# Kernel tuning notes

Hardware: AMD Instinct MI355X
Metric: run time of the kernel (lower is better)

Reference implementation:

```python
import jax, jax.numpy as jnp
import numpy as np

N_NODES = 10000
N_EDGES = 160000
MUL = 64            # multiplicity of 0e and 1o in node features
AVG_NEIGH = 16.0    # avg_num_neighbors
N_BESSEL = 8
NUM_IRREPS = 4 * MUL  # 2*MUL scalars (0e) + 2*MUL vectors (1o) after concat+regroup

# e3nn normalize2mom constant for swish: 1/sqrt(E_{z~N(0,1)}[swish(z)^2])
_z, _w = np.polynomial.hermite_e.hermegauss(128)
_silu = _z / (1.0 + np.exp(-_z))
ACT_C = float(1.0 / np.sqrt(np.sum(_w * _silu ** 2) / np.sqrt(2.0 * np.pi)))


def bessel(x, n=N_BESSEL):
    # e3nn.bessel with x_max=1: sqrt(2) * sin(k*pi*x)/x, k=1..n
    k = jnp.arange(1, n + 1, dtype=x.dtype)
    xs = jnp.where(x == 0.0, 1.0, x)[:, None]
    return jnp.sqrt(2.0) * jnp.where(x[:, None] == 0.0, k * jnp.pi, jnp.sin(jnp.pi * k * xs) / xs)


def envelope(x):
    return jnp.where(x < 1.0, 1.0 - 28.0 * x ** 6 + 48.0 * x ** 7 - 21.0 * x ** 8, 0.0)


def mlp(x, Ws):
    # e3nn MultiLayerPerceptron: y = x @ W / sqrt(fan_in), normalized swish on hidden layers
    n = len(Ws)
    for i, W in enumerate(Ws):
        x = x @ W / jnp.sqrt(jnp.asarray(W.shape[0], x.dtype))
        if i < n - 1:
            x = ACT_C * jax.nn.swish(x)
    return x


def setup_inputs() -> dict:
    key = jax.random.key(0)
    ks = jax.random.split(key, 8)
    vectors = 0.35 * jax.random.normal(ks[0], (N_EDGES, 3), jnp.float32)
    node_scalars = jax.random.normal(ks[1], (N_NODES, MUL), jnp.float32)
    node_vectors = jax.random.normal(ks[2], (N_NODES, MUL, 3), jnp.float32)
    senders = jax.random.randint(ks[3], (N_EDGES,), 0, N_NODES)
    receivers = jax.random.randint(ks[4], (N_EDGES,), 0, N_NODES)
    W1 = jax.random.normal(ks[5], (N_BESSEL, 64), jnp.float32)
    W2 = jax.random.normal(ks[6], (64, 64), jnp.float32)
    W3 = jax.random.normal(ks[7], (64, NUM_IRREPS), jnp.float32)
    return dict(vectors=vectors, node_scalars=node_scalars, node_vectors=node_vectors,
                senders=senders, receivers=receivers, W1=W1, W2=W2, W3=W3)


def reference(vectors, node_scalars, node_vectors, senders, receivers, W1, W2, W3):
    lengths = jnp.linalg.norm(vectors, axis=-1, keepdims=True)        # [E,1]
    Y1 = jnp.sqrt(3.0) * vectors / lengths                            # component-normalized l=1 SH [E,3]

    # gather sender features
    m0 = node_scalars[senders]                                        # [E,MUL]   0e
    m1 = node_vectors[senders]                                        # [E,MUL,3] 1o

    # CG tensor product with Y1, filtered to target irreps (0e + 1o), component norm
    tp0 = jnp.einsum('eui,ei->eu', m1, Y1) / jnp.sqrt(3.0)            # 1o x 1o -> 0e
    tp1 = m0[:, :, None] * Y1[:, None, :]                             # 0e x 1o -> 1o

    s = jnp.concatenate([m0, tp0], axis=1)                            # [E,2*MUL]
    v = jnp.concatenate([m1, tp1], axis=1)                            # [E,2*MUL,3]

    # radial embedding -> per-irrep gates
    x = lengths[:, 0]
    radial = bessel(x) * envelope(x)[:, None]                         # [E,8]
    mix = mlp(radial, (W1, W2, W3))                                   # [E,4*MUL]

    s = s * mix[:, : 2 * MUL]
    v = v * mix[:, 2 * MUL :, None]

    # scatter-add to receivers
    out_s = jax.ops.segment_sum(s, receivers, num_segments=N_NODES)   # [N,2*MUL]
    out_v = jax.ops.segment_sum(v, receivers, num_segments=N_NODES)   # [N,2*MUL,3]
    inv = 1.0 / jnp.sqrt(AVG_NEIGH)
    return jnp.concatenate([out_s * inv, (out_v * inv).reshape(N_NODES, -1)], axis=1)
```

## Files before the change

### kernel.cpp

```cpp
#include <hip/hip_runtime.h>
#include <hip/hip_fp16.h>
#include <math.h>

#define N_NODES 10000
#define N_EDGES 160000
#define TBL_N 512
#define ACT_C 1.676518f
#define CAP 64
#define S3 1.7320508075688772f

#define SCAT_BLOCKS 625
#define CONV_BLOCKS 2500
#define TBL_BLOCKS  129

__device__ uint4  g_tblp[TBL_N * 64];
__device__ uint2  g_nd2[N_NODES * 64];
__device__ int    g_cnt[N_NODES];
__device__ float4 g_bkt[N_NODES * CAP];

__device__ __forceinline__ float2 h2f(unsigned int v) {
    __half2 h = *(__half2*)&v;
    return __half22float2(h);
}

__global__ __launch_bounds__(256) void prep_scatter(
    const float* __restrict__ W1, const float* __restrict__ W2, const float* __restrict__ W3,
    const float* __restrict__ node_scalars, const float* __restrict__ node_vectors,
    const float* __restrict__ vectors, const int* __restrict__ senders,
    const int* __restrict__ receivers)
{
    const int bx = (int)blockIdx.x;
    const int tid = threadIdx.x;
    const int lane = tid & 63;
    const int wl = tid >> 6;

    if (bx < SCAT_BLOCKS) {
        int e = bx * 256 + tid;
        if (e < N_EDGES) {
            float vx = vectors[3 * e], vy = vectors[3 * e + 1], vz = vectors[3 * e + 2];
            float x2 = vx * vx + vy * vy + vz * vz;
            if (x2 < 1.0f) {
                float invx = rsqrtf(x2);
                float x = x2 * invx;
                float t = x * (float)TBL_N;
                int idx = (int)t;            if (idx > TBL_N - 1) idx = TBL_N - 1;
                int fr  = (int)((t - (float)idx) * 512.0f);  if (fr > 511) fr = 511;
                unsigned int bits = ((unsigned int)senders[e] << 18) |
                                    ((unsigned int)idx << 9) | (unsigned int)fr;
                int r = receivers[e];
                int slot = atomicAdd(&g_cnt[r], 1);
                if (slot < CAP)
                    g_bkt[(r << 6) + slot] =
                        make_float4(vx * invx, vy * invx, vz * invx, __uint_as_float(bits));
            }
        }
        return;
    }
    if (bx < SCAT_BLOCKS + CONV_BLOCKS) {
        int n = (bx - SCAT_BLOCKS) * 4 + wl;
        float m0 = node_scalars[n * 64 + lane];
        const float* p = node_vectors + n * 192 + 3 * lane;
        __half2 h01 = __floats2half2_rn(m0, p[0]);
        __half2 h23 = __floats2half2_rn(p[1], p[2]);
        uint2 r;
        r.x = *(unsigned int*)&h01;
        r.y = *(unsigned int*)&h23;
        g_nd2[n * 64 + lane] = r;
        return;
    }

    __shared__ float h[4][64];
    int wid = (bx - SCAT_BLOCKS - CONV_BLOCKS) * 4 + wl;
    if (wid > TBL_N) wid = TBL_N;
    const float x = (float)wid * (1.0f / (float)TBL_N);
    float x2 = x * x, x3 = x2 * x, x6 = x3 * x3;
    float env = (x < 1.0f) ? (1.0f - 28.0f * x6 + 48.0f * x6 * x - 21.0f * x6 * x2) : 0.0f;
    const float pi = 3.14159265358979f;
    float radial[8];
    #pragma unroll
    for (int k = 1; k <= 8; ++k) {
        float b = (x == 0.0f) ? ((float)k * pi) : (sinf(pi * (float)k * x) / x);
        radial[k - 1] = 1.41421356237f * b * env;
    }
    float acc = 0.0f;
    #pragma unroll
    for (int k = 0; k < 8; ++k) acc += radial[k] * W1[k * 64 + lane];
    acc *= 0.35355339059f;
    float a = ACT_C * acc / (1.0f + expf(-acc));
    h[wl][lane] = a;
    __syncthreads();
    acc = 0.0f;
    #pragma unroll 8
    for (int k = 0; k < 64; ++k) acc += h[wl][k] * W2[k * 64 + lane];
    acc *= 0.125f;
    a = ACT_C * acc / (1.0f + expf(-acc));
    __syncthreads();
    h[wl][lane] = a;
    __syncthreads();
    float m0 = 0.f, m1 = 0.f, m2 = 0.f, m3 = 0.f;
    #pragma unroll 4
    for (int k = 0; k < 64; ++k) {
        float hk = h[wl][k];
        const float* w = W3 + k * 256 + lane;
        m0 += hk * w[0];
        m1 += hk * w[64];
        m2 += hk * w[128];
        m3 += hk * w[192];
    }
    __half2 h01 = __floats2half2_rn(m0 * 0.125f, m1 * 0.125f);
    __half2 h23 = __floats2half2_rn(m2 * 0.125f, m3 * 0.125f);
    uint2 r;
    r.x = *(unsigned int*)&h01;
    r.y = *(unsigned int*)&h23;
    if (wid < TBL_N) *(uint2*)&g_tblp[wid * 64 + lane] = r;
    if (wid >= 1)    *(uint2*)((char*)&g_tblp[(wid - 1) * 64 + lane] + 8) = r;
}

__device__ __forceinline__ void edge_body(int j, const float4& myrec,
                                          int u, float& accA, float& accB,
                                          float& aCx, float& aCy, float& aCz,
                                          float& aDx, float& aDy, float& aDz) {
    float yx = __shfl(myrec.x, j);
    float yy = __shfl(myrec.y, j);
    float yz = __shfl(myrec.z, j);
    unsigned int bits = __float_as_uint(__shfl(myrec.w, j));
    int sv = (int)(bits >> 18);
    int i  = (int)((bits >> 9) & 511u);
    float f = (float)(bits & 511u) * (1.0f / 512.0f);

    uint4 q  = g_tblp[i * 64 + u];
    uint2 nv = g_nd2[sv * 64 + u];

    float2 a0 = h2f(q.x);
    float2 b0 = h2f(q.y);
    float2 a1 = h2f(q.z);
    float2 b1 = h2f(q.w);
    float2 p01 = h2f(nv.x);
    float2 p23 = h2f(nv.y);

    float mA = fmaf(f, a1.x - a0.x, a0.x);
    float mB = fmaf(f, a1.y - a0.y, a0.y);
    float mC = fmaf(f, b1.x - b0.x, b0.x);
    float mD = fmaf(f, b1.y - b0.y, b0.y);

    float m0u = p01.x, vx = p01.y, vy = p23.x, vzv = p23.y;
    float tp0 = fmaf(vx, yx, fmaf(vy, yy, vzv * yz));
    accA = fmaf(m0u, mA, accA);
    accB = fmaf(tp0, mB, accB);
    aCx = fmaf(mC, vx,  aCx);
    aCy = fmaf(mC, vy,  aCy);
    aCz = fmaf(mC, vzv, aCz);
    float cD = m0u * mD * S3;
    aDx = fmaf(cD, yx, aDx);
    aDy = fmaf(cD, yy, aDy);
    aDz = fmaf(cD, yz, aDz);
}

__global__ __launch_bounds__(256) void gather_kernel(float* __restrict__ out) {
    __shared__ float smem[3][8][64];
    const int n = (int)blockIdx.x;
    const int u = threadIdx.x & 63;
    const int w = threadIdx.x >> 6;

    int cnt = g_cnt[n]; if (cnt > CAP) cnt = CAP;
    int ql = (cnt + 3) >> 2;
    int beg = w * ql;
    int len = cnt - beg; if (len > ql) len = ql; if (len < 0) len = 0;
    const int base = n << 6;
    const float4 myrec = g_bkt[base + beg + (u < len ? u : 0)];

    float accA = 0.f, accB = 0.f;
    float aCx = 0.f, aCy = 0.f, aCz = 0.f;
    float aDx = 0.f, aDy = 0.f, aDz = 0.f;
    int j = 0;
    for (; j + 2 <= len; j += 2) {
        edge_body(j,     myrec, u, accA, accB, aCx, aCy, aCz, aDx, aDy, aDz);
        edge_body(j + 1, myrec, u, accA, accB, aCx, aCy, aCz, aDx, aDy, aDz);
    }
    if (j < len)
        edge_body(j,     myrec, u, accA, accB, aCx, aCy, aCz, aDx, aDy, aDz);

    if (w > 0) {
        smem[w - 1][0][u] = accA;  smem[w - 1][1][u] = accB;
        smem[w - 1][2][u] = aCx;   smem[w - 1][3][u] = aCy;
        smem[w - 1][4][u] = aCz;   smem[w - 1][5][u] = aDx;
        smem[w - 1][6][u] = aDy;   smem[w - 1][7][u] = aDz;
    }
    __syncthreads();
    if (w == 0) {
        #pragma unroll
        for (int s = 0; s < 3; ++s) {
            accA += smem[s][0][u]; accB += smem[s][1][u];
            aCx  += smem[s][2][u]; aCy  += smem[s][3][u];
            aCz  += smem[s][4][u]; aDx  += smem[s][5][u];
            aDy  += smem[s][6][u]; aDz  += smem[s][7][u];
        }
        const float inv = 0.25f;
        float* o = out + (size_t)n * 512;
        o[u]       = inv * accA;
        o[64 + u]  = inv * accB;
        o[128 + 3 * u + 0] = inv * aCx;
        o[128 + 3 * u + 1] = inv * aCy;
        o[128 + 3 * u + 2] = inv * aCz;
        o[320 + 3 * u + 0] = inv * aDx;
        o[320 + 3 * u + 1] = inv * aDy;
        o[320 + 3 * u + 2] = inv * aDz;
    }
    if (threadIdx.x == 0) g_cnt[n] = 0;
}

extern "C" void kernel_launch(void* const* d_in, const int* in_sizes, int n_in,
                              void* d_out, int out_size, void* d_ws, size_t ws_size,
                              hipStream_t stream) {
    const float* vectors      = (const float*)d_in[0];
    const float* node_scalars = (const float*)d_in[1];
    const float* node_vectors = (const float*)d_in[2];
    const int*   senders      = (const int*)d_in[3];
    const int*   receivers    = (const int*)d_in[4];
    const float* W1           = (const float*)d_in[5];
    const float* W2           = (const float*)d_in[6];
    const float* W3           = (const float*)d_in[7];
    float* out = (float*)d_out;

    prep_scatter<<<SCAT_BLOCKS + CONV_BLOCKS + TBL_BLOCKS, 256, 0, stream>>>(
        W1, W2, W3, node_scalars, node_vectors, vectors, senders, receivers);
    gather_kernel<<<N_NODES, 256, 0, stream>>>(out);
}
```

Baseline: 43.60 us.

## Stage coarser radial table in LDS and gather nodes per wave persistently

Shrinks the radial-MLP interpolation table to 127 entries stored as plain uint2 and copies it into shared memory in each block of a persistent gather kernel. Each wave now handles one whole node, removing the cross-wave shared-memory reduction, and edge loads are batched four at a time to expose memory-level parallelism. Sender bits are repacked to fit the smaller index field. The trade-offs are coarser interpolation accuracy, a per-block table copy, and a large LDS footprint that limits occupancy.

After: 45.29 us. +3.9%, slower.

```diff
diff --git a/kernel.cpp b/kernel.cpp
--- a/kernel.cpp
+++ b/kernel.cpp
@@ -4,16 +4,18 @@
 
 #define N_NODES 10000
 #define N_EDGES 160000
-#define TBL_N 512
+#define TBL_N 126
 #define ACT_C 1.676518f
 #define CAP 64
 #define S3 1.7320508075688772f
 
 #define SCAT_BLOCKS 625
 #define CONV_BLOCKS 2500
-#define TBL_BLOCKS  129
-
-__device__ uint4  g_tblp[TBL_N * 64];
+#define TBL_BLOCKS  32
+#define GATHER_BLOCKS 512
+#define GATHER_THREADS 512
+
+__device__ uint2  g_tbl[(TBL_N + 1) * 64];
 __device__ uint2  g_nd2[N_NODES * 64];
 __device__ int    g_cnt[N_NODES];
 __device__ float4 g_bkt[N_NODES * CAP];
@@ -45,7 +47,7 @@
                 float t = x * (float)TBL_N;
                 int idx = (int)t;            if (idx > TBL_N - 1) idx = TBL_N - 1;
                 int fr  = (int)((t - (float)idx) * 512.0f);  if (fr > 511) fr = 511;
-                unsigned int bits = ((unsigned int)senders[e] << 18) |
+                unsigned int bits = ((unsigned int)senders[e] << 16) |
                                     ((unsigned int)idx << 9) | (unsigned int)fr;
                 int r = receivers[e];
                 int slot = atomicAdd(&g_cnt[r], 1);
@@ -112,29 +114,18 @@
     uint2 r;
     r.x = *(unsigned int*)&h01;
     r.y = *(unsigned int*)&h23;
-    if (wid < TBL_N) *(uint2*)&g_tblp[wid * 64 + lane] = r;
-    if (wid >= 1)    *(uint2*)((char*)&g_tblp[(wid - 1) * 64 + lane] + 8) = r;
-}
-
-__device__ __forceinline__ void edge_body(int j, const float4& myrec,
-                                          int u, float& accA, float& accB,
+    g_tbl[wid * 64 + lane] = r;
+}
+
+__device__ __forceinline__ void edge_math(uint2 q0, uint2 q1, uint2 nv, float f,
+                                          float yx, float yy, float yz,
+                                          float& accA, float& accB,
                                           float& aCx, float& aCy, float& aCz,
                                           float& aDx, float& aDy, float& aDz) {
-    float yx = __shfl(myrec.x, j);
-    float yy = __shfl(myrec.y, j);
-    float yz = __shfl(myrec.z, j);
-    unsigned int bits = __float_as_uint(__shfl(myrec.w, j));
-    int sv = (int)(bits >> 18);
-    int i  = (int)((bits >> 9) & 511u);
-    float f = (float)(bits & 511u) * (1.0f / 512.0f);
-
-    uint4 q  = g_tblp[i * 64 + u];
-    uint2 nv = g_nd2[sv * 64 + u];
-
-    float2 a0 = h2f(q.x);
-    float2 b0 = h2f(q.y);
-    float2 a1 = h2f(q.z);
-    float2 b1 = h2f(q.w);
+    float2 a0 = h2f(q0.x);
+    float2 b0 = h2f(q0.y);
+    float2 a1 = h2f(q1.x);
+    float2 b1 = h2f(q1.y);
     float2 p01 = h2f(nv.x);
     float2 p23 = h2f(nv.y);
 
@@ -156,45 +147,61 @@
     aDz = fmaf(cD, yz, aDz);
 }
 
-__global__ __launch_bounds__(256) void gather_kernel(float* __restrict__ out) {
-    __shared__ float smem[3][8][64];
-    const int n = (int)blockIdx.x;
-    const int u = threadIdx.x & 63;
-    const int w = threadIdx.x >> 6;
-
-    int cnt = g_cnt[n]; if (cnt > CAP) cnt = CAP;
-    int ql = (cnt + 3) >> 2;
-    int beg = w * ql;
-    int len = cnt - beg; if (len > ql) len = ql; if (len < 0) len = 0;
-    const int base = n << 6;
-    const float4 myrec = g_bkt[base + beg + (u < len ? u : 0)];
-
-    float accA = 0.f, accB = 0.f;
-    float aCx = 0.f, aCy = 0.f, aCz = 0.f;
-    float aDx = 0.f, aDy = 0.f, aDz = 0.f;
-    int j = 0;
-    for (; j + 2 <= len; j += 2) {
-        edge_body(j,     myrec, u, accA, accB, aCx, aCy, aCz, aDx, aDy, aDz);
-        edge_body(j + 1, myrec, u, accA, accB, aCx, aCy, aCz, aDx, aDy, aDz);
-    }
-    if (j < len)
-        edge_body(j,     myrec, u, accA, accB, aCx, aCy, aCz, aDx, aDy, aDz);
-
-    if (w > 0) {
-        smem[w - 1][0][u] = accA;  smem[w - 1][1][u] = accB;
-        smem[w - 1][2][u] = aCx;   smem[w - 1][3][u] = aCy;
-        smem[w - 1][4][u] = aCz;   smem[w - 1][5][u] = aDx;
-        smem[w - 1][6][u] = aDy;   smem[w - 1][7][u] = aDz;
-    }
-    __syncthreads();
-    if (w == 0) {
-        #pragma unroll
-        for (int s = 0; s < 3; ++s) {
-            accA += smem[s][0][u]; accB += smem[s][1][u];
-            aCx  += smem[s][2][u]; aCy  += smem[s][3][u];
-            aCz  += smem[s][4][u]; aDx  += smem[s][5][u];
-            aDy  += smem[s][6][u]; aDz  += smem[s][7][u];
+__global__ __launch_bounds__(GATHER_THREADS) void gather_kernel(float* __restrict__ out) {
+    __shared__ uint2 tbl[(TBL_N + 1) * 64];
+    const int tid = threadIdx.x;
+    for (int i = tid; i < (TBL_N + 1) * 64; i += GATHER_THREADS)
+        tbl[i] = g_tbl[i];
+    __syncthreads();
+
+    const int u = tid & 63;
+    const int w = tid >> 6;
+    const int nwaves = GATHER_BLOCKS * 8;
+
+    for (int n = (int)blockIdx.x * 8 + w; n < N_NODES; n += nwaves) {
+        int cnt = g_cnt[n]; if (cnt > CAP) cnt = CAP;
+        const int base = n << 6;
+        const float4 myrec = g_bkt[base + (u < cnt ? u : 0)];
+
+        float accA = 0.f, accB = 0.f;
+        float aCx = 0.f, aCy = 0.f, aCz = 0.f;
+        float aDx = 0.f, aDy = 0.f, aDz = 0.f;
+
+        int j = 0;
+        for (; j + 4 <= cnt; j += 4) {
+            uint2 q0[4], q1[4], nv[4];
+            float yx[4], yy[4], yz[4], f[4];
+            #pragma unroll
+            for (int k = 0; k < 4; ++k) {
+                int jj = j + k;
+                yx[k] = __shfl(myrec.x, jj);
+                yy[k] = __shfl(myrec.y, jj);
+                yz[k] = __shfl(myrec.z, jj);
+                unsigned int bits = __float_as_uint(__shfl(myrec.w, jj));
+                int sv = (int)(bits >> 16);
+                int i  = (int)((bits >> 9) & 127u);
+                f[k] = (float)(bits & 511u) * (1.0f / 512.0f);
+                q0[k] = tbl[i * 64 + u];
+                q1[k] = tbl[i * 64 + 64 + u];
+                nv[k] = g_nd2[sv * 64 + u];
+            }
+            #pragma unroll
+            for (int k = 0; k < 4; ++k)
+                edge_math(q0[k], q1[k], nv[k], f[k], yx[k], yy[k], yz[k],
+                          accA, accB, aCx, aCy, aCz, aDx, aDy, aDz);
         }
+        for (; j < cnt; ++j) {
+            float yx = __shfl(myrec.x, j);
+            float yy = __shfl(myrec.y, j);
+            float yz = __shfl(myrec.z, j);
+            unsigned int bits = __float_as_uint(__shfl(myrec.w, j));
+            int sv = (int)(bits >> 16);
+            int i  = (int)((bits >> 9) & 127u);
+            float f = (float)(bits & 511u) * (1.0f / 512.0f);
+            edge_math(tbl[i * 64 + u], tbl[i * 64 + 64 + u], g_nd2[sv * 64 + u], f,
+                      yx, yy, yz, accA, accB, aCx, aCy, aCz, aDx, aDy, aDz);
+        }
+
         const float inv = 0.25f;
         float* o = out + (size_t)n * 512;
         o[u]       = inv * accA;
@@ -205,8 +212,8 @@
         o[320 + 3 * u + 0] = inv * aDx;
         o[320 + 3 * u + 1] = inv * aDy;
         o[320 + 3 * u + 2] = inv * aDz;
-    }
-    if (threadIdx.x == 0) g_cnt[n] = 0;
+        if (u == 0) g_cnt[n] = 0;
+    }
 }
 
 extern "C" void kernel_launch(void* const* d_in, const int* in_sizes, int n_in,
@@ -224,5 +231,5 @@
 
     prep_scatter<<<SCAT_BLOCKS + CONV_BLOCKS + TBL_BLOCKS, 256, 0, stream>>>(
         W1, W2, W3, node_scalars, node_vectors, vectors, senders, receivers);
-    gather_kernel<<<N_NODES, 256, 0, stream>>>(out);
-}
+    gather_kernel<<<GATHER_BLOCKS, GATHER_THREADS, 0, stream>>>(out);
+}
```
